# Optimization experiments

Hardware: AMD Instinct MI355X
Metric: run time of the kernel (lower is better)

The kernel has to match this reference:

```python
import jax, jax.numpy as jnp
import numpy as np

F = 64
PASS_STEPS = 3
VAR_N, CON_N, EQ_N = 50000, 50000, 10000
NNZ, EQ_NNZ = 800000, 200000
CONT_SCALE = 0.1  # continuous_var_scale


def _pairnorm(x):
    # PairNorm(subtract_mean=False): x / sqrt(mean_i ||x_i||^2 + eps)
    return x / jnp.sqrt(1e-6 + jnp.mean(jnp.sum(x * x, axis=1)))


def _mlp(x, w1, b1, w2, b2):
    # Linear -> PairNorm -> ReLU -> Linear (fused elementwise chain)
    return jax.nn.relu(_pairnorm(x @ w1 + b1)) @ w2 + b2


def _segsum(vals, idx, n):
    return jax.ops.segment_sum(vals, idx, num_segments=n)


def setup_inputs() -> dict:
    key = jax.random.key(0)
    ks = jax.random.split(key, 32)
    def w(k, i, o):
        return jax.random.normal(k, (i, o), jnp.float32) / np.sqrt(i).astype(np.float32)
    z = lambda n: jnp.zeros((n,), jnp.float32)
    return {
        "ineq_src": jax.random.randint(ks[0], (NNZ,), 0, VAR_N),
        "ineq_dst": jax.random.randint(ks[1], (NNZ,), 0, CON_N),
        "ineq_val": jax.random.normal(ks[2], (NNZ,), jnp.float32),
        "eq_src": jax.random.randint(ks[3], (EQ_NNZ,), 0, VAR_N),
        "eq_dst": jax.random.randint(ks[4], (EQ_NNZ,), 0, EQ_N),
        "eq_val": jax.random.normal(ks[5], (EQ_NNZ,), jnp.float32),
        "const_values": jax.random.normal(ks[6], (CON_N,), jnp.float32),
        "eq_const_values": jax.random.normal(ks[7], (EQ_N,), jnp.float32),
        "relaxed_solution": jax.random.uniform(ks[8], (VAR_N,), jnp.float32),
        "objective_multipliers": jax.random.normal(ks[9], (VAR_N,), jnp.float32),
        "integer_mask": (jax.random.uniform(ks[10], (VAR_N,)) < 0.5).astype(jnp.float32),
        "noise": jax.random.normal(ks[11], (PASS_STEPS, VAR_N, 4), jnp.float32),
        "q_w1": w(ks[12], F + 4, F), "q_b1": z(F),
        "q_w2": w(ks[13], F, F), "q_b2": z(F),
        "cu_w1": w(ks[14], 2 * F, F), "cu_b1": z(F),
        "cu_w2": w(ks[15], F, 2 * F), "cu_b2": z(2 * F),
        "ec_w1": w(ks[16], 2 * F, F), "ec_b1": z(F),
        "ec_w2": w(ks[17], F, 2 * F), "ec_b2": z(2 * F),
        "vu_w1": w(ks[18], 4 * F + 2, F), "vu_b1": z(F),
        "vu_w2": w(ks[19], F, F), "vu_b2": z(F),
        "o_w1": w(ks[20], F, F), "o_b1": z(F),
        "o_w2": w(ks[21], F, 1), "o_b2": z(1),
    }


def reference(ineq_src, ineq_dst, ineq_val, eq_src, eq_dst, eq_val,
              const_values, eq_const_values, relaxed_solution,
              objective_multipliers, integer_mask, noise,
              q_w1, q_b1, q_w2, q_b2, cu_w1, cu_b1, cu_w2, cu_b2,
              ec_w1, ec_b1, ec_w2, ec_b2, vu_w1, vu_b1, vu_w2, vu_b2,
              o_w1, o_b1, o_w2, o_b2):
    var_n = relaxed_solution.shape[0]
    con_n = const_values.shape[0]
    eq_n = eq_const_values.shape[0]
    f = q_w2.shape[1]
    cv = const_values[:, None]
    ecv = eq_const_values[:, None]
    int_mask = integer_mask[:, None]
    obj = objective_multipliers[:, None]
    obj = obj / (jnp.sqrt(jnp.mean(obj * obj)) + 1e-6)

    variables = jnp.ones((var_n, f), ineq_val.dtype) * relaxed_solution[:, None]
    # A^T @ variables and B^T @ variables (bipartite SpMM as gather + segment-sum)
    constraints = _segsum(ineq_val[:, None] * variables[ineq_src], ineq_dst, con_n)
    eq_constraints = _segsum(eq_val[:, None] * variables[eq_src], eq_dst, eq_n)

    val_pos = jax.nn.relu(ineq_val)
    val_neg = jax.nn.relu(-ineq_val)
    const_scaler = jnp.sqrt(_segsum(ineq_val ** 2, ineq_dst, con_n) + 1e-6)[:, None]
    eq_scaler = jnp.sqrt(_segsum(eq_val ** 2, eq_dst, eq_n) + 1e-6)[:, None]
    vars_scaler = jnp.sqrt(_segsum(ineq_val ** 2, ineq_src, var_n) + 1e-6)[:, None]

    outputs = []
    for i in range(noise.shape[0]):  # pass_steps, small fixed count
        query = _mlp(jnp.concatenate([variables, noise[i]], axis=-1), q_w1, q_b1, q_w2, q_b2)
        query = query + 0.5 * int_mask  # (q+0.5)*m + q*(1-m)

        lhs = _segsum(ineq_val[:, None] * query[ineq_src], ineq_dst, con_n)
        const_loss = (lhs - cv) / const_scaler
        const_tmp = _mlp(jnp.concatenate([constraints, const_loss], axis=-1), cu_w1, cu_b1, cu_w2, cu_b2)
        constraints = const_tmp[:, :f] + 0.5 * constraints
        cf = const_tmp[:, f:]
        msg_pos = _segsum(val_pos[:, None] * cf[ineq_dst], ineq_src, var_n) / vars_scaler
        msg_neg = _segsum(val_neg[:, None] * cf[ineq_dst], ineq_src, var_n) / vars_scaler

        eq_lhs = _segsum(eq_val[:, None] * query[eq_src], eq_dst, eq_n)
        eq_loss = jnp.square((ecv - eq_lhs) / eq_scaler)
        eq_tmp = _mlp(jnp.concatenate([eq_constraints, eq_loss], axis=-1), ec_w1, ec_b1, ec_w2, ec_b2)
        eq_constraints = eq_tmp[:, :f] + 0.5 * eq_constraints
        eq2var = _segsum(eq_val[:, None] * eq_tmp[:, f:][eq_dst], eq_src, var_n)

        var_msg = jnp.concatenate([variables, msg_pos, msg_neg, eq2var, obj, int_mask], axis=-1)
        variables = _mlp(var_msg, vu_w1, vu_b1, vu_w2, vu_b2) + 0.5 * variables

        out_vars = _mlp(variables, o_w1, o_b1, o_w2, o_b2)
        # eval mode: no logistic noise injected
        out = jax.nn.sigmoid(out_vars) * int_mask + out_vars * (1.0 - int_mask) * CONT_SCALE
        outputs.append(out)

    return jnp.stack(outputs), out_vars
```

## Files before the change

kernel.cpp:

```cpp
#include <hip/hip_runtime.h>
#include <hip/hip_fp16.h>
#include <math.h>


constexpr int VAR_N = 50000;
constexpr int CON_N = 50000;
constexpr int EQ_N  = 10000;
constexpr int NNZ_I = 800000;
constexpr int NNZ_E = 200000;
constexpr int NPASS = 3;

constexpr int CAP_ID = 48;
constexpr int CAP_IS = 48;
constexpr int CAP_ED = 64;
constexpr int CAP_ES = 24;

typedef _Float16 f16x8 __attribute__((ext_vector_type(8)));
typedef float    f32x4 __attribute__((ext_vector_type(4)));

__device__ __forceinline__ float wred(float v) {
#pragma unroll
  for (int o = 32; o > 0; o >>= 1) v += __shfl_down(v, o, 64);
  return v;
}

__device__ __forceinline__ float unpack_val(unsigned e) {
  return __half2float(__ushort_as_half((unsigned short)(e & 0xFFFFu)));
}

__device__ __forceinline__ unsigned u4get(const uint4& q, int k) {
  return k == 0 ? q.x : (k == 1 ? q.y : (k == 2 ? q.z : q.w));
}

__device__ __forceinline__ float cellsum(const float* p) {
  float s = 0.0f;
#pragma unroll
  for (int i = 0; i < 8; ++i) s += p[i * 16];
  return s;
}

struct PrepArgs {
  const float* src[9];
  int K[9]; int C[9]; int base[9]; int end[9];
};

__global__ __launch_bounds__(256) void prep_wt_k(PrepArgs a, __half* __restrict__ wt)
{
  int idx = blockIdx.x * 256 + threadIdx.x;
  if (idx >= 65536) return;
#pragma unroll
  for (int i = 0; i < 9; ++i) {
    if (idx < a.end[i]) {
      int local = idx - a.base[i];
      int k = local % a.K[i];
      int c = local / a.K[i];
      wt[idx] = __float2half_rn(a.src[i][(size_t)k * a.C[i] + c]);
      return;
    }
  }
}

struct GemmSide {
  const float* X0; const float* X1;
  const __half* WT;
  const float* W;  const float* bias;
  float* out; float* aux;
  const float* ssin; float* ssout; float ssdiv;
  const float* exA; const float* exB; const float* exScale;
  int N; int nblk;
};

template<int K, int COLS, int MODE, int EXTRA, bool RELUNORM, bool OUT_SS, int POSTOP>
__global__ __launch_bounds__(256) void mlp_gemm(GemmSide A, GemmSide B)
{
  constexpr int NCB = COLS / 16;
  constexpr int NS  = K / 32;
  constexpr int KP  = K + 8;
  __shared__ __half Wl[COLS * KP];
  __shared__ float red[4];

  const bool inA = (blockIdx.x < (unsigned)A.nblk);
  const GemmSide& S = inA ? A : B;
  const int bid = blockIdx.x - (inA ? 0 : A.nblk);
  const int nblk = inA ? A.nblk : B.nblk;

  const int tid = threadIdx.x, lane = tid & 63, wid = tid >> 6;
  const int lr = lane & 15;
  const int kgrp = (lane >> 4) * 8;

  for (int idx = tid; idx < COLS * (K / 8); idx += 256) {
    int c = idx / (K / 8), seg = idx % (K / 8);
    *(f16x8*)&Wl[c * KP + seg * 8] = *(const f16x8*)(S.WT + (size_t)c * K + seg * 8);
  }
  __syncthreads();

  float inv_s = 1.0f;
  if constexpr (RELUNORM) inv_s = rsqrtf(1e-6f + cellsum(S.ssin) / S.ssdiv);
  float oscale = 0.0f;
  if constexpr (EXTRA == 2) oscale = 1.0f / (sqrtf((*S.exScale) * (1.0f / VAR_N)) + 1e-6f);

  float bcol[NCB], ew0[NCB], ew1[NCB], ew2[NCB], ew3[NCB];
#pragma unroll
  for (int c = 0; c < NCB; ++c) {
    int col = c * 16 + lr;
    bcol[c] = S.bias[col];
    if constexpr (EXTRA == 1) {
      ew0[c] = S.W[(size_t)(K + 0) * COLS + col];
      ew1[c] = S.W[(size_t)(K + 1) * COLS + col];
      ew2[c] = S.W[(size_t)(K + 2) * COLS + col];
      ew3[c] = S.W[(size_t)(K + 3) * COLS + col];
    }
    if constexpr (EXTRA == 2) {
      ew0[c] = S.W[(size_t)(K + 0) * COLS + col];
      ew1[c] = S.W[(size_t)(K + 1) * COLS + col];
    }
  }

  const int nStrips = (S.N + 15) / 16;
  const int nw = nblk * 4;
  float ssloc = 0.0f;

  for (int strip = bid * 4 + wid; strip < nStrips; strip += nw) {
    const int row0 = strip * 16;
    const int arow = row0 + lr;
    const bool rok = arow < S.N;

    float4 u[NS], v[NS];
#pragma unroll
    for (int s = 0; s < NS; ++s) {
      if (rok) {
        const int gk = s * 32 + kgrp;
        const float* p;
        if constexpr (MODE == 0) p = S.X0 + (size_t)arow * K + gk;
        else p = (gk < 64) ? (S.X0 + ((size_t)arow << 6) + gk)
                           : (S.X1 + (size_t)arow * (K - 64) + (gk - 64));
        u[s] = *(const float4*)p;
        v[s] = *(const float4*)(p + 4);
      } else {
        u[s] = make_float4(0.f, 0.f, 0.f, 0.f);
        v[s] = make_float4(0.f, 0.f, 0.f, 0.f);
      }
    }

    f32x4 acc[NCB] = {};
#pragma unroll
    for (int s = 0; s < NS; ++s) {
      float4 uu = u[s], vv = v[s];
      if constexpr (RELUNORM) {
        uu.x = fmaxf(uu.x, 0.f); uu.y = fmaxf(uu.y, 0.f);
        uu.z = fmaxf(uu.z, 0.f); uu.w = fmaxf(uu.w, 0.f);
        vv.x = fmaxf(vv.x, 0.f); vv.y = fmaxf(vv.y, 0.f);
        vv.z = fmaxf(vv.z, 0.f); vv.w = fmaxf(vv.w, 0.f);
      }
      f16x8 af;
      af[0] = (_Float16)uu.x; af[1] = (_Float16)uu.y;
      af[2] = (_Float16)uu.z; af[3] = (_Float16)uu.w;
      af[4] = (_Float16)vv.x; af[5] = (_Float16)vv.y;
      af[6] = (_Float16)vv.z; af[7] = (_Float16)vv.w;
#pragma unroll
      for (int c = 0; c < NCB; ++c) {
        const f16x8 bf = *(const f16x8*)&Wl[(c * 16 + lr) * KP + s * 32 + kgrp];
        acc[c] = __builtin_amdgcn_mfma_f32_16x16x32_f16(af, bf, acc[c], 0, 0, 0);
      }
    }

#pragma unroll
    for (int j = 0; j < 4; ++j) {
      int grow = row0 + ((lane >> 4) << 2) + j;
      if (grow < S.N) {
        float nx = 0, ny = 0, nz = 0, nw4 = 0, ov = 0, mv = 0;
        if constexpr (EXTRA == 1) {
          float4 n4 = *reinterpret_cast<const float4*>(&S.exA[(size_t)grow * 4]);
          nx = n4.x; ny = n4.y; nz = n4.z; nw4 = n4.w;
        }
        if constexpr (EXTRA == 2) { ov = S.exA[grow] * oscale; mv = S.exB[grow]; }
#pragma unroll
        for (int c = 0; c < NCB; ++c) {
          int col = c * 16 + lr;
          float vv2 = acc[c][j];
          if constexpr (RELUNORM) vv2 *= inv_s;
          vv2 += bcol[c];
          if constexpr (EXTRA == 1)
            vv2 = fmaf(nx, ew0[c], fmaf(ny, ew1[c], fmaf(nz, ew2[c], fmaf(nw4, ew3[c], vv2))));
          if constexpr (EXTRA == 2)
            vv2 = fmaf(ov, ew0[c], fmaf(mv, ew1[c], vv2));
          if constexpr (POSTOP == 1) vv2 += 0.5f * S.aux[grow];
          if constexpr (POSTOP == 2) vv2 += 0.5f * S.aux[((size_t)grow << 6) + col];
          if constexpr (POSTOP == 3) {
            if (col < 64) {
              float nv = vv2 + 0.5f * S.aux[((size_t)grow << 6) + col];
              S.aux[((size_t)grow << 6) + col] = nv;
            } else {
              S.out[((size_t)grow << 6) + (col - 64)] = vv2;
            }
          } else {
            S.out[(size_t)grow * COLS + col] = vv2;
          }
          if constexpr (OUT_SS) ssloc = fmaf(vv2, vv2, ssloc);
        }
      }
    }
  }

  if constexpr (OUT_SS) {
    ssloc = wred(ssloc);
    if (lane == 0) red[wid] = ssloc;
    __syncthreads();
    if (tid == 0) {
      float s = red[0] + red[1] + red[2] + red[3];
      atomicAdd(&S.ssout[(blockIdx.x & 7) * 16], s);
    }
  }
}

constexpr int QI = NNZ_I / 4;
constexpr int QE = NNZ_E / 4;

__global__ __launch_bounds__(256) void build_all_k(
    const int* __restrict__ isrc, const int* __restrict__ idst, const float* __restrict__ ival,
    const int* __restrict__ esrc, const int* __restrict__ edst, const float* __restrict__ evalv,
    int* __restrict__ cntID, unsigned* __restrict__ listID,
    int* __restrict__ cntIS, unsigned* __restrict__ listIS,
    int* __restrict__ cntED, unsigned* __restrict__ listED,
    int* __restrict__ cntES, unsigned* __restrict__ listES)
{
  int t = blockIdx.x * 256 + threadIdx.x;
  if (t < QI) {
    int4   s4 = *(const int4*)(isrc + 4 * t);
    int4   d4 = *(const int4*)(idst + 4 * t);
    float4 v4 = *(const float4*)(ival + 4 * t);
    int   ss[4] = { s4.x, s4.y, s4.z, s4.w };
    int   dd[4] = { d4.x, d4.y, d4.z, d4.w };
    float vv[4] = { v4.x, v4.y, v4.z, v4.w };
    unsigned hb[4]; int pd[4], ps[4];
#pragma unroll
    for (int k = 0; k < 4; ++k) hb[k] = (unsigned)__half_as_ushort(__float2half_rn(vv[k]));
#pragma unroll
    for (int k = 0; k < 4; ++k) pd[k] = atomicAdd(&cntID[dd[k]], 1);
#pragma unroll
    for (int k = 0; k < 4; ++k) ps[k] = atomicAdd(&cntIS[ss[k]], 1);
#pragma unroll
    for (int k = 0; k < 4; ++k)
      if (pd[k] < CAP_ID) listID[(size_t)dd[k] * CAP_ID + pd[k]] = ((unsigned)ss[k] << 16) | hb[k];
#pragma unroll
    for (int k = 0; k < 4; ++k)
      if (ps[k] < CAP_IS) listIS[(size_t)ss[k] * CAP_IS + ps[k]] = ((unsigned)dd[k] << 16) | hb[k];
  } else if (t < QI + QE) {
    int e = t - QI;
    int4   s4 = *(const int4*)(esrc + 4 * e);
    int4   d4 = *(const int4*)(edst + 4 * e);
    float4 v4 = *(const float4*)(evalv + 4 * e);
    int   ss[4] = { s4.x, s4.y, s4.z, s4.w };
    int   dd[4] = { d4.x, d4.y, d4.z, d4.w };
    float vv[4] = { v4.x, v4.y, v4.z, v4.w };
    unsigned hb[4]; int pd[4], ps[4];
#pragma unroll
    for (int k = 0; k < 4; ++k) hb[k] = (unsigned)__half_as_ushort(__float2half_rn(vv[k]));
#pragma unroll
    for (int k = 0; k < 4; ++k) pd[k] = atomicAdd(&cntED[dd[k]], 1);
#pragma unroll
    for (int k = 0; k < 4; ++k) ps[k] = atomicAdd(&cntES[ss[k]], 1);
#pragma unroll
    for (int k = 0; k < 4; ++k)
      if (pd[k] < CAP_ED) listED[(size_t)dd[k] * CAP_ED + pd[k]] = ((unsigned)ss[k] << 16) | hb[k];
#pragma unroll
    for (int k = 0; k < 4; ++k)
      if (ps[k] < CAP_ES) listES[(size_t)ss[k] * CAP_ES + ps[k]] = ((unsigned)dd[k] << 16) | hb[k];
  }
}

__global__ __launch_bounds__(256) void init_rows_k(
    const float* __restrict__ relaxed,
    const int* __restrict__ cntID, const unsigned* __restrict__ listID,
    const int* __restrict__ cntED, const unsigned* __restrict__ listED,
    float* __restrict__ variables, float* __restrict__ constraints, float* __restrict__ eqcons)
{
  int widx = blockIdx.x * 4 + (threadIdx.x >> 6);
  int lane = threadIdx.x & 63;
  if (widx < VAR_N) {
    variables[((size_t)widx << 6) + lane] = relaxed[widx];
  } else if (widx < VAR_N + CON_N) {
    int i = widx - VAR_N;
    int n = min(cntID[i], CAP_ID);
    float t = 0.0f;
    if (lane < n) {
      unsigned e = listID[(size_t)i * CAP_ID + lane];
      t = unpack_val(e) * relaxed[e >> 16];
    }
    t = wred(t);
    t = __shfl(t, 0, 64);
    constraints[((size_t)i << 6) + lane] = t;
  } else if (widx < VAR_N + CON_N + EQ_N) {
    int i = widx - VAR_N - CON_N;
    int n = min(cntED[i], CAP_ED);
    float t = 0.0f;
    if (lane < n) {
      unsigned e = listED[(size_t)i * CAP_ED + lane];
      t = unpack_val(e) * relaxed[e >> 16];
    }
    t = wred(t);
    t = __shfl(t, 0, 64);
    eqcons[((size_t)i << 6) + lane] = t;
  }
}

__global__ __launch_bounds__(256) void gather_loss_k(
    const int* __restrict__ cntC, const unsigned* __restrict__ listC,
    const int* __restrict__ cntE, const unsigned* __restrict__ listE,
    const float* __restrict__ qry,
    const float* __restrict__ cv, const float* __restrict__ ecv,
    float* __restrict__ closs, float* __restrict__ eloss)
{
  constexpr int nbC = (CON_N + 3) / 4;
  int b = blockIdx.x;
  int lane = threadIdx.x & 63;
  if (b < nbC) {
    int i = b * 4 + (threadIdx.x >> 6);
    if (i >= CON_N) return;
    int n = min(cntC[i], CAP_ID);
    const uint4* lst = (const uint4*)(listC + (size_t)i * CAP_ID);
    float acc = 0.0f, ss = 0.0f;
    for (int j4 = 0; j4 * 4 < n; ++j4) {
      uint4 q = lst[j4];
#pragma unroll
      for (int k = 0; k < 4; ++k) {
        int j = j4 * 4 + k;
        if (j < n) {
          unsigned e = u4get(q, k);
          float v = unpack_val(e);
          acc = fmaf(v, qry[((size_t)(e >> 16) << 6) + lane], acc);
          ss  = fmaf(v, v, ss);
        }
      }
    }
    closs[((size_t)i << 6) + lane] = (acc - cv[i]) * rsqrtf(ss + 1e-6f);
  } else {
    int i = (b - nbC) * 4 + (threadIdx.x >> 6);
    if (i >= EQ_N) return;
    int n = min(cntE[i], CAP_ED);
    const uint4* lst = (const uint4*)(listE + (size_t)i * CAP_ED);
    float acc = 0.0f, ss = 0.0f;
    for (int j4 = 0; j4 * 4 < n; ++j4) {
      uint4 q = lst[j4];
#pragma unroll
      for (int k = 0; k < 4; ++k) {
        int j = j4 * 4 + k;
        if (j < n) {
          unsigned e = u4get(q, k);
          float v = unpack_val(e);
          acc = fmaf(v, qry[((size_t)(e >> 16) << 6) + lane], acc);
          ss  = fmaf(v, v, ss);
        }
      }
    }
    float t = (ecv[i] - acc) * rsqrtf(ss + 1e-6f);
    eloss[((size_t)i << 6) + lane] = t * t;
  }
}

__global__ __launch_bounds__(256) void gather_vmsg_k(
    const int* __restrict__ cntS, const unsigned* __restrict__ listS,
    const int* __restrict__ cntES, const unsigned* __restrict__ listES,
    const float* __restrict__ ctmpHi, const float* __restrict__ etmpHi,
    float* __restrict__ msgs)
{
  int i = blockIdx.x * 4 + (threadIdx.x >> 6);
  if (i >= VAR_N) return;
  int lane = threadIdx.x & 63;

  float pos = 0.0f, neg = 0.0f, vss = 0.0f;
  {
    int n = min(cntS[i], CAP_IS);
    const uint4* lst = (const uint4*)(listS + (size_t)i * CAP_IS);
    for (int j4 = 0; j4 * 4 < n; ++j4) {
      uint4 q = lst[j4];
#pragma unroll
      for (int k = 0; k < 4; ++k) {
        int j = j4 * 4 + k;
        if (j < n) {
          unsigned e = u4get(q, k);
          float v = unpack_val(e);
          float c = ctmpHi[((size_t)(e >> 16) << 6) + lane];
          vss = fmaf(v, v, vss);
          if (v > 0.0f) pos = fmaf(v, c, pos);
          else          neg = fmaf(-v, c, neg);
        }
      }
    }
  }
  float e2v = 0.0f;
  {
    int n = min(cntES[i], CAP_ES);
    const uint4* lst = (const uint4*)(listES + (size_t)i * CAP_ES);
    for (int j4 = 0; j4 * 4 < n; ++j4) {
      uint4 q = lst[j4];
#pragma unroll
      for (int k = 0; k < 4; ++k) {
        int j = j4 * 4 + k;
        if (j < n) {
          unsigned e = u4get(q, k);
          e2v = fmaf(unpack_val(e), etmpHi[((size_t)(e >> 16) << 6) + lane], e2v);
        }
      }
    }
  }
  float ivs = rsqrtf(vss + 1e-6f);
  float* row = msgs + (size_t)i * 192;
  row[lane]       = pos * ivs;
  row[64 + lane]  = neg * ivs;
  row[128 + lane] = e2v;
}

__global__ __launch_bounds__(256) void sumsq_k(const float* __restrict__ x, int n, float* out)
{
  float s = 0.0f;
  for (int i = blockIdx.x * 256 + threadIdx.x; i < n; i += gridDim.x * 256) {
    float v = x[i]; s = fmaf(v, v, s);
  }
  s = wred(s);
  __shared__ float red[4];
  int lane = threadIdx.x & 63, wid = threadIdx.x >> 6;
  if (lane == 0) red[wid] = s;
  __syncthreads();
  if (threadIdx.x == 0) atomicAdd(out, red[0] + red[1] + red[2] + red[3]);
}

__global__ __launch_bounds__(256) void out_k(
    const float* __restrict__ H, const float* __restrict__ ssin,
    const float* __restrict__ ow2, const float* __restrict__ ob2,
    const float* __restrict__ mask, float* __restrict__ dout, int pass)
{
  int row = blockIdx.x * 4 + (threadIdx.x >> 6);
  if (row >= VAR_N) return;
  int lane = threadIdx.x & 63;
  float inv_s = rsqrtf(1e-6f + cellsum(ssin) / (float)VAR_N);
  float t = fmaxf(H[(size_t)row * 64 + lane] * inv_s, 0.0f) * ow2[lane];
  t = wred(t);
  if (lane == 0) {
    float ov = t + ob2[0];
    float m = mask[row];
    float sig = 1.0f / (1.0f + expf(-ov));
    dout[pass * VAR_N + row] = sig * m + ov * (1.0f - m) * 0.1f;
    if (pass == NPASS - 1) dout[3 * VAR_N + row] = ov;
  }
}

extern "C" void kernel_launch(void* const* d_in, const int* in_sizes, int n_in,
                              void* d_out, int out_size, void* d_ws, size_t ws_size,
                              hipStream_t stream)
{
  const int*   isrc = (const int*)  d_in[0];
  const int*   idst = (const int*)  d_in[1];
  const float* ival = (const float*)d_in[2];
  const int*   esrc = (const int*)  d_in[3];
  const int*   edst = (const int*)  d_in[4];
  const float* evalv= (const float*)d_in[5];
  const float* cv   = (const float*)d_in[6];
  const float* ecv  = (const float*)d_in[7];
  const float* relaxed = (const float*)d_in[8];
  const float* obj  = (const float*)d_in[9];
  const float* mask = (const float*)d_in[10];
  const float* noise= (const float*)d_in[11];
  const float* q_w1 = (const float*)d_in[12];
  const float* q_b1 = (const float*)d_in[13];
  const float* q_w2 = (const float*)d_in[14];
  const float* q_b2 = (const float*)d_in[15];
  const float* cu_w1= (const float*)d_in[16];
  const float* cu_b1= (const float*)d_in[17];
  const float* cu_w2= (const float*)d_in[18];
  const float* cu_b2= (const float*)d_in[19];
  const float* ec_w1= (const float*)d_in[20];
  const float* ec_b1= (const float*)d_in[21];
  const float* ec_w2= (const float*)d_in[22];
  const float* ec_b2= (const float*)d_in[23];
  const float* vu_w1= (const float*)d_in[24];
  const float* vu_b1= (const float*)d_in[25];
  const float* vu_w2= (const float*)d_in[26];
  const float* vu_b2= (const float*)d_in[27];
  const float* o_w1 = (const float*)d_in[28];
  const float* o_b1 = (const float*)d_in[29];
  const float* o_w2 = (const float*)d_in[30];
  const float* o_b2 = (const float*)d_in[31];
  float* dout = (float*)d_out;
  float* w = (float*)d_ws;

  size_t off = 0;
  auto A = [&](size_t n){ size_t o = off; off += (n + 63) & ~(size_t)63; return o; };
  const size_t oVarA  = A((size_t)VAR_N * 64);
  const size_t oVarB  = A((size_t)VAR_N * 64);
  const size_t oCons  = A((size_t)CON_N * 64);
  const size_t oEqc   = A((size_t)EQ_N  * 64);
  const size_t oQry   = A((size_t)VAR_N * 64);
  const size_t oH     = A((size_t)VAR_N * 64);
  const size_t oHE    = A((size_t)EQ_N  * 64);
  const size_t oCtmp  = A((size_t)CON_N * 64);
  const size_t oEtmp  = A((size_t)EQ_N  * 64);
  const size_t oCloss = A((size_t)CON_N * 64);
  const size_t oEloss = A((size_t)EQ_N  * 64);
  const size_t oMsgs  = A((size_t)VAR_N * 192);
  const size_t oScal  = A(2048);
  const size_t oWT    = A(32768);
  const size_t oCntID = A(CON_N);
  const size_t oCntIS = A(VAR_N);
  const size_t oCntED = A(EQ_N);
  const size_t oCntES = A(VAR_N);
  const size_t oListID = A((size_t)CON_N * CAP_ID);
  const size_t oListIS = A((size_t)VAR_N * CAP_IS);
  const size_t oListED = A((size_t)EQ_N  * CAP_ED);
  const size_t oListES = A((size_t)VAR_N * CAP_ES);

  float* scal = w + oScal;
  __half* wtBase = (__half*)(w + oWT);
  int*  cntID = (int*)(w + oCntID);
  int*  cntIS = (int*)(w + oCntIS);
  int*  cntED = (int*)(w + oCntED);
  int*  cntES = (int*)(w + oCntES);
  unsigned* listID = (unsigned*)(w + oListID);
  unsigned* listIS = (unsigned*)(w + oListIS);
  unsigned* listED = (unsigned*)(w + oListED);
  unsigned* listES = (unsigned*)(w + oListES);

  const int bQ1 = 0,      bQ2 = 4096,  bCU1 = 8192,  bCU2 = 16384, bEC1 = 24576;
  const int bEC2 = 32768, bVU1 = 40960, bVU2 = 57344, bO1 = 61440;

  hipMemsetAsync((void*)(w + oScal), 0, 2048 * 4, stream);
  hipMemsetAsync((void*)(w + oCntID), 0, (oListID - oCntID) * 4, stream);

  {
    PrepArgs pa;
    const float* srcs[9] = { q_w1, q_w2, cu_w1, cu_w2, ec_w1, ec_w2, vu_w1, vu_w2, o_w1 };
    int Ks[9]   = { 64, 64, 128, 64, 128, 64, 256, 64, 64 };
    int Cs[9]   = { 64, 64, 64, 128, 64, 128, 64, 64, 64 };
    int bases[9]= { bQ1, bQ2, bCU1, bCU2, bEC1, bEC2, bVU1, bVU2, bO1 };
    for (int i = 0; i < 9; ++i) {
      pa.src[i] = srcs[i]; pa.K[i] = Ks[i]; pa.C[i] = Cs[i];
      pa.base[i] = bases[i]; pa.end[i] = bases[i] + Ks[i] * Cs[i];
    }
    prep_wt_k<<<(65536 + 255) / 256, 256, 0, stream>>>(pa, wtBase);
  }

  build_all_k<<<(QI + QE + 255) / 256, 256, 0, stream>>>(
      isrc, idst, ival, esrc, edst, evalv,
      cntID, listID, cntIS, listIS, cntED, listED, cntES, listES);
  sumsq_k<<<64, 256, 0, stream>>>(obj, VAR_N, scal);
  init_rows_k<<<(VAR_N + CON_N + EQ_N + 3) / 4, 256, 0, stream>>>(
      relaxed, cntID, listID, cntED, listED, w + oVarA, w + oCons, w + oEqc);

  float* varCur = w + oVarA;
  float* varNxt = w + oVarB;

  GemmSide Z = {};
  const int NBV = 768;
  const int NBC = 640, NBE = 128;

  for (int p = 0; p < NPASS; ++p) {
    float* ssq0 = scal + 16 + (size_t)(p * 5 + 0) * 128;
    float* ssq1 = scal + 16 + (size_t)(p * 5 + 1) * 128;
    float* ssq2 = scal + 16 + (size_t)(p * 5 + 2) * 128;
    float* ssq3 = scal + 16 + (size_t)(p * 5 + 3) * 128;
    float* ssq4 = scal + 16 + (size_t)(p * 5 + 4) * 128;

    {
      GemmSide S = { varCur, nullptr, wtBase + bQ1, q_w1, q_b1, w + oH, nullptr,
                     nullptr, ssq0, 1.0f,
                     noise + (size_t)p * VAR_N * 4, nullptr, nullptr, VAR_N, NBV };
      mlp_gemm<64, 64, 0, 1, false, true, 0><<<NBV, 256, 0, stream>>>(S, Z);
    }
    {
      GemmSide S = { w + oH, nullptr, wtBase + bQ2, q_w2, q_b2, w + oQry, (float*)mask,
                     ssq0, nullptr, (float)VAR_N,
                     nullptr, nullptr, nullptr, VAR_N, NBV };
      mlp_gemm<64, 64, 0, 0, true, false, 1><<<NBV, 256, 0, stream>>>(S, Z);
    }
    gather_loss_k<<<(CON_N + 3) / 4 + (EQ_N + 3) / 4, 256, 0, stream>>>(
        cntID, listID, cntED, listED, w + oQry, cv, ecv, w + oCloss, w + oEloss);
    {
      GemmSide Sa = { w + oCons, w + oCloss, wtBase + bCU1, cu_w1, cu_b1, w + oH, nullptr,
                      nullptr, ssq1, 1.0f, nullptr, nullptr, nullptr, CON_N, NBC };
      GemmSide Sb = { w + oEqc, w + oEloss, wtBase + bEC1, ec_w1, ec_b1, w + oHE, nullptr,
                      nullptr, ssq2, 1.0f, nullptr, nullptr, nullptr, EQ_N, NBE };
      mlp_gemm<128, 64, 1, 0, false, true, 0><<<NBC + NBE, 256, 0, stream>>>(Sa, Sb);
    }
    {
      GemmSide Sa = { w + oH, nullptr, wtBase + bCU2, cu_w2, cu_b2, w + oCtmp, w + oCons,
                      ssq1, nullptr, (float)CON_N, nullptr, nullptr, nullptr, CON_N, NBC };
      GemmSide Sb = { w + oHE, nullptr, wtBase + bEC2, ec_w2, ec_b2, w + oEtmp, w + oEqc,
                      ssq2, nullptr, (float)EQ_N, nullptr, nullptr, nullptr, EQ_N, NBE };
      mlp_gemm<64, 128, 0, 0, true, false, 3><<<NBC + NBE, 256, 0, stream>>>(Sa, Sb);
    }
    gather_vmsg_k<<<(VAR_N + 3) / 4, 256, 0, stream>>>(
        cntIS, listIS, cntES, listES, w + oCtmp, w + oEtmp, w + oMsgs);
    {
      GemmSide S = { varCur, w + oMsgs, wtBase + bVU1, vu_w1, vu_b1, w + oH, nullptr,
                     nullptr, ssq3, 1.0f, obj, mask, scal, VAR_N, NBV };
      mlp_gemm<256, 64, 1, 2, false, true, 0><<<NBV, 256, 0, stream>>>(S, Z);
    }
    {
      GemmSide S = { w + oH, nullptr, wtBase + bVU2, vu_w2, vu_b2, varNxt, varCur,
                     ssq3, nullptr, (float)VAR_N, nullptr, nullptr, nullptr, VAR_N, NBV };
      mlp_gemm<64, 64, 0, 0, true, false, 2><<<NBV, 256, 0, stream>>>(S, Z);
    }
    {
      GemmSide S = { varNxt, nullptr, wtBase + bO1, o_w1, o_b1, w + oH, nullptr,
                     nullptr, ssq4, 1.0f, nullptr, nullptr, nullptr, VAR_N, NBV };
      mlp_gemm<64, 64, 0, 0, false, true, 0><<<NBV, 256, 0, stream>>>(S, Z);
    }
    out_k<<<(VAR_N + 3) / 4, 256, 0, stream>>>(w + oH, ssq4, o_w2, o_b2, mask, dout, p);

    float* t = varCur; varCur = varNxt; varNxt = t;
  }
}
```

Baseline: 1.040 ms.

## Store all intermediate activations in fp16 to halve memory traffic

Changes every intermediate activation buffer (variables, constraints, queries, hidden layers, messages, losses) from fp32 to fp16, so GEMM kernels load f16x8 directly into MFMA operands and the gather kernels read half-width rows. The aim is to cut the bandwidth of the memory-bound gathers and GEMM loads. The edge-list build kernel also changes from four to two edges per thread. The cost is lower precision in the recurrent state and possible overflow or underflow in the fp16 intermediates.

```diff
diff --git a/kernel.cpp b/kernel.cpp
--- a/kernel.cpp
+++ b/kernel.cpp
@@ -17,6 +17,7 @@
 
 typedef _Float16 f16x8 __attribute__((ext_vector_type(8)));
 typedef float    f32x4 __attribute__((ext_vector_type(4)));
+typedef _Float16 half_t;
 
 __device__ __forceinline__ float wred(float v) {
 #pragma unroll
@@ -44,7 +45,7 @@
   int K[9]; int C[9]; int base[9]; int end[9];
 };
 
-__global__ __launch_bounds__(256) void prep_wt_k(PrepArgs a, __half* __restrict__ wt)
+__global__ __launch_bounds__(256) void prep_wt_k(PrepArgs a, half_t* __restrict__ wt)
 {
   int idx = blockIdx.x * 256 + threadIdx.x;
   if (idx >= 65536) return;
@@ -54,17 +55,17 @@
       int local = idx - a.base[i];
       int k = local % a.K[i];
       int c = local / a.K[i];
-      wt[idx] = __float2half_rn(a.src[i][(size_t)k * a.C[i] + c]);
+      wt[idx] = (half_t)a.src[i][(size_t)k * a.C[i] + c];
       return;
     }
   }
 }
 
 struct GemmSide {
-  const float* X0; const float* X1;
-  const __half* WT;
+  const half_t* X0; const half_t* X1;
+  const half_t* WT;
   const float* W;  const float* bias;
-  float* out; float* aux;
+  half_t* out; half_t* auxH; const float* auxF;
   const float* ssin; float* ssout; float ssdiv;
   const float* exA; const float* exB; const float* exScale;
   int N; int nblk;
@@ -76,7 +77,7 @@
   constexpr int NCB = COLS / 16;
   constexpr int NS  = K / 32;
   constexpr int KP  = K + 8;
-  __shared__ __half Wl[COLS * KP];
+  __shared__ half_t Wl[COLS * KP];
   __shared__ float red[4];
 
   const bool inA = (blockIdx.x < (unsigned)A.nblk);
@@ -125,42 +126,33 @@
     const int arow = row0 + lr;
     const bool rok = arow < S.N;
 
-    float4 u[NS], v[NS];
+    f16x8 af[NS];
 #pragma unroll
     for (int s = 0; s < NS; ++s) {
       if (rok) {
         const int gk = s * 32 + kgrp;
-        const float* p;
+        const half_t* p;
         if constexpr (MODE == 0) p = S.X0 + (size_t)arow * K + gk;
         else p = (gk < 64) ? (S.X0 + ((size_t)arow << 6) + gk)
                            : (S.X1 + (size_t)arow * (K - 64) + (gk - 64));
-        u[s] = *(const float4*)p;
-        v[s] = *(const float4*)(p + 4);
+        af[s] = *(const f16x8*)p;
       } else {
-        u[s] = make_float4(0.f, 0.f, 0.f, 0.f);
-        v[s] = make_float4(0.f, 0.f, 0.f, 0.f);
+        af[s] = f16x8{0, 0, 0, 0, 0, 0, 0, 0};
       }
     }
 
     f32x4 acc[NCB] = {};
 #pragma unroll
     for (int s = 0; s < NS; ++s) {
-      float4 uu = u[s], vv = v[s];
+      f16x8 a = af[s];
       if constexpr (RELUNORM) {
-        uu.x = fmaxf(uu.x, 0.f); uu.y = fmaxf(uu.y, 0.f);
-        uu.z = fmaxf(uu.z, 0.f); uu.w = fmaxf(uu.w, 0.f);
-        vv.x = fmaxf(vv.x, 0.f); vv.y = fmaxf(vv.y, 0.f);
-        vv.z = fmaxf(vv.z, 0.f); vv.w = fmaxf(vv.w, 0.f);
-      }
-      f16x8 af;
-      af[0] = (_Float16)uu.x; af[1] = (_Float16)uu.y;
-      af[2] = (_Float16)uu.z; af[3] = (_Float16)uu.w;
-      af[4] = (_Float16)vv.x; af[5] = (_Float16)vv.y;
-      af[6] = (_Float16)vv.z; af[7] = (_Float16)vv.w;
+#pragma unroll
+        for (int i = 0; i < 8; ++i) a[i] = a[i] > (half_t)0 ? a[i] : (half_t)0;
+      }
 #pragma unroll
       for (int c = 0; c < NCB; ++c) {
         const f16x8 bf = *(const f16x8*)&Wl[(c * 16 + lr) * KP + s * 32 + kgrp];
-        acc[c] = __builtin_amdgcn_mfma_f32_16x16x32_f16(af, bf, acc[c], 0, 0, 0);
+        acc[c] = __builtin_amdgcn_mfma_f32_16x16x32_f16(a, bf, acc[c], 0, 0, 0);
       }
     }
 
@@ -184,17 +176,17 @@
             vv2 = fmaf(nx, ew0[c], fmaf(ny, ew1[c], fmaf(nz, ew2[c], fmaf(nw4, ew3[c], vv2))));
           if constexpr (EXTRA == 2)
             vv2 = fmaf(ov, ew0[c], fmaf(mv, ew1[c], vv2));
-          if constexpr (POSTOP == 1) vv2 += 0.5f * S.aux[grow];
-          if constexpr (POSTOP == 2) vv2 += 0.5f * S.aux[((size_t)grow << 6) + col];
+          if constexpr (POSTOP == 1) vv2 += 0.5f * S.auxF[grow];
+          if constexpr (POSTOP == 2) vv2 += 0.5f * (float)S.auxH[((size_t)grow << 6) + col];
           if constexpr (POSTOP == 3) {
             if (col < 64) {
-              float nv = vv2 + 0.5f * S.aux[((size_t)grow << 6) + col];
-              S.aux[((size_t)grow << 6) + col] = nv;
+              float nv = vv2 + 0.5f * (float)S.auxH[((size_t)grow << 6) + col];
+              S.auxH[((size_t)grow << 6) + col] = (half_t)nv;
             } else {
-              S.out[((size_t)grow << 6) + (col - 64)] = vv2;
+              S.out[((size_t)grow << 6) + (col - 64)] = (half_t)vv2;
             }
           } else {
-            S.out[(size_t)grow * COLS + col] = vv2;
+            S.out[(size_t)grow * COLS + col] = (half_t)vv2;
           }
           if constexpr (OUT_SS) ssloc = fmaf(vv2, vv2, ssloc);
         }
@@ -213,8 +205,8 @@
   }
 }
 
-constexpr int QI = NNZ_I / 4;
-constexpr int QE = NNZ_E / 4;
+constexpr int QI2 = NNZ_I / 2;
+constexpr int QE2 = NNZ_E / 2;
 
 __global__ __launch_bounds__(256) void build_all_k(
     const int* __restrict__ isrc, const int* __restrict__ idst, const float* __restrict__ ival,
@@ -225,46 +217,46 @@
     int* __restrict__ cntES, unsigned* __restrict__ listES)
 {
   int t = blockIdx.x * 256 + threadIdx.x;
-  if (t < QI) {
-    int4   s4 = *(const int4*)(isrc + 4 * t);
-    int4   d4 = *(const int4*)(idst + 4 * t);
-    float4 v4 = *(const float4*)(ival + 4 * t);
-    int   ss[4] = { s4.x, s4.y, s4.z, s4.w };
-    int   dd[4] = { d4.x, d4.y, d4.z, d4.w };
-    float vv[4] = { v4.x, v4.y, v4.z, v4.w };
-    unsigned hb[4]; int pd[4], ps[4];
-#pragma unroll
-    for (int k = 0; k < 4; ++k) hb[k] = (unsigned)__half_as_ushort(__float2half_rn(vv[k]));
-#pragma unroll
-    for (int k = 0; k < 4; ++k) pd[k] = atomicAdd(&cntID[dd[k]], 1);
-#pragma unroll
-    for (int k = 0; k < 4; ++k) ps[k] = atomicAdd(&cntIS[ss[k]], 1);
-#pragma unroll
-    for (int k = 0; k < 4; ++k)
+  if (t < QI2) {
+    int2   s2 = *(const int2*)(isrc + 2 * t);
+    int2   d2 = *(const int2*)(idst + 2 * t);
+    float2 v2 = *(const float2*)(ival + 2 * t);
+    int   ss[2] = { s2.x, s2.y };
+    int   dd[2] = { d2.x, d2.y };
+    float vv[2] = { v2.x, v2.y };
+    unsigned hb[2]; int pd[2], ps[2];
+#pragma unroll
+    for (int k = 0; k < 2; ++k) hb[k] = (unsigned)__half_as_ushort(__float2half_rn(vv[k]));
+#pragma unroll
+    for (int k = 0; k < 2; ++k) pd[k] = atomicAdd(&cntID[dd[k]], 1);
+#pragma unroll
+    for (int k = 0; k < 2; ++k) ps[k] = atomicAdd(&cntIS[ss[k]], 1);
+#pragma unroll
+    for (int k = 0; k < 2; ++k)
       if (pd[k] < CAP_ID) listID[(size_t)dd[k] * CAP_ID + pd[k]] = ((unsigned)ss[k] << 16) | hb[k];
 #pragma unroll
-    for (int k = 0; k < 4; ++k)
+    for (int k = 0; k < 2; ++k)
       if (ps[k] < CAP_IS) listIS[(size_t)ss[k] * CAP_IS + ps[k]] = ((unsigned)dd[k] << 16) | hb[k];
-  } else if (t < QI + QE) {
-    int e = t - QI;
-    int4   s4 = *(const int4*)(esrc + 4 * e);
-    int4   d4 = *(const int4*)(edst + 4 * e);
-    float4 v4 = *(const float4*)(evalv + 4 * e);
-    int   ss[4] = { s4.x, s4.y, s4.z, s4.w };
-    int   dd[4] = { d4.x, d4.y, d4.z, d4.w };
-    float vv[4] = { v4.x, v4.y, v4.z, v4.w };
-    unsigned hb[4]; int pd[4], ps[4];
-#pragma unroll
-    for (int k = 0; k < 4; ++k) hb[k] = (unsigned)__half_as_ushort(__float2half_rn(vv[k]));
-#pragma unroll
-    for (int k = 0; k < 4; ++k) pd[k] = atomicAdd(&cntED[dd[k]], 1);
-#pragma unroll
-    for (int k = 0; k < 4; ++k) ps[k] = atomicAdd(&cntES[ss[k]], 1);
-#pragma unroll
-    for (int k = 0; k < 4; ++k)
+  } else if (t < QI2 + QE2) {
+    int e = t - QI2;
+    int2   s2 = *(const int2*)(esrc + 2 * e);
+    int2   d2 = *(const int2*)(edst + 2 * e);
+    float2 v2 = *(const float2*)(evalv + 2 * e);
+    int   ss[2] = { s2.x, s2.y };
+    int   dd[2] = { d2.x, d2.y };
+    float vv[2] = { v2.x, v2.y };
+    unsigned hb[2]; int pd[2], ps[2];
+#pragma unroll
+    for (int k = 0; k < 2; ++k) hb[k] = (unsigned)__half_as_ushort(__float2half_rn(vv[k]));
+#pragma unroll
+    for (int k = 0; k < 2; ++k) pd[k] = atomicAdd(&cntED[dd[k]], 1);
+#pragma unroll
+    for (int k = 0; k < 2; ++k) ps[k] = atomicAdd(&cntES[ss[k]], 1);
+#pragma unroll
+    for (int k = 0; k < 2; ++k)
       if (pd[k] < CAP_ED) listED[(size_t)dd[k] * CAP_ED + pd[k]] = ((unsigned)ss[k] << 16) | hb[k];
 #pragma unroll
-    for (int k = 0; k < 4; ++k)
+    for (int k = 0; k < 2; ++k)
       if (ps[k] < CAP_ES) listES[(size_t)ss[k] * CAP_ES + ps[k]] = ((unsigned)dd[k] << 16) | hb[k];
   }
 }
@@ -273,12 +265,12 @@
     const float* __restrict__ relaxed,
     const int* __restrict__ cntID, const unsigned* __restrict__ listID,
     const int* __restrict__ cntED, const unsigned* __restrict__ listED,
-    float* __restrict__ variables, float* __restrict__ constraints, float* __restrict__ eqcons)
+    half_t* __restrict__ variables, half_t* __restrict__ constraints, half_t* __restrict__ eqcons)
 {
   int widx = blockIdx.x * 4 + (threadIdx.x >> 6);
   int lane = threadIdx.x & 63;
   if (widx < VAR_N) {
-    variables[((size_t)widx << 6) + lane] = relaxed[widx];
+    variables[((size_t)widx << 6) + lane] = (half_t)relaxed[widx];
   } else if (widx < VAR_N + CON_N) {
     int i = widx - VAR_N;
     int n = min(cntID[i], CAP_ID);
@@ -289,7 +281,7 @@
     }
     t = wred(t);
     t = __shfl(t, 0, 64);
-    constraints[((size_t)i << 6) + lane] = t;
+    constraints[((size_t)i << 6) + lane] = (half_t)t;
   } else if (widx < VAR_N + CON_N + EQ_N) {
     int i = widx - VAR_N - CON_N;
     int n = min(cntED[i], CAP_ED);
@@ -300,16 +292,16 @@
     }
     t = wred(t);
     t = __shfl(t, 0, 64);
-    eqcons[((size_t)i << 6) + lane] = t;
+    eqcons[((size_t)i << 6) + lane] = (half_t)t;
   }
 }
 
 __global__ __launch_bounds__(256) void gather_loss_k(
     const int* __restrict__ cntC, const unsigned* __restrict__ listC,
     const int* __restrict__ cntE, const unsigned* __restrict__ listE,
-    const float* __restrict__ qry,
+    const half_t* __restrict__ qry,
     const float* __restrict__ cv, const float* __restrict__ ecv,
-    float* __restrict__ closs, float* __restrict__ eloss)
+    half_t* __restrict__ closs, half_t* __restrict__ eloss)
 {
   constexpr int nbC = (CON_N + 3) / 4;
   int b = blockIdx.x;
@@ -328,12 +320,12 @@
         if (j < n) {
           unsigned e = u4get(q, k);
           float v = unpack_val(e);
-          acc = fmaf(v, qry[((size_t)(e >> 16) << 6) + lane], acc);
+          acc = fmaf(v, (float)qry[((size_t)(e >> 16) << 6) + lane], acc);
           ss  = fmaf(v, v, ss);
         }
       }
     }
-    closs[((size_t)i << 6) + lane] = (acc - cv[i]) * rsqrtf(ss + 1e-6f);
+    closs[((size_t)i << 6) + lane] = (half_t)((acc - cv[i]) * rsqrtf(ss + 1e-6f));
   } else {
     int i = (b - nbC) * 4 + (threadIdx.x >> 6);
     if (i >= EQ_N) return;
@@ -348,21 +340,21 @@
         if (j < n) {
           unsigned e = u4get(q, k);
           float v = unpack_val(e);
-          acc = fmaf(v, qry[((size_t)(e >> 16) << 6) + lane], acc);
+          acc = fmaf(v, (float)qry[((size_t)(e >> 16) << 6) + lane], acc);
           ss  = fmaf(v, v, ss);
         }
       }
     }
     float t = (ecv[i] - acc) * rsqrtf(ss + 1e-6f);
-    eloss[((size_t)i << 6) + lane] = t * t;
+    eloss[((size_t)i << 6) + lane] = (half_t)(t * t);
   }
 }
 
 __global__ __launch_bounds__(256) void gather_vmsg_k(
     const int* __restrict__ cntS, const unsigned* __restrict__ listS,
     const int* __restrict__ cntES, const unsigned* __restrict__ listES,
-    const float* __restrict__ ctmpHi, const float* __restrict__ etmpHi,
-    float* __restrict__ msgs)
+    const half_t* __restrict__ ctmpHi, const half_t* __restrict__ etmpHi,
+    half_t* __restrict__ msgs)
 {
   int i = blockIdx.x * 4 + (threadIdx.x >> 6);
   if (i >= VAR_N) return;
@@ -380,7 +372,7 @@
         if (j < n) {
           unsigned e = u4get(q, k);
           float v = unpack_val(e);
-          float c = ctmpHi[((size_t)(e >> 16) << 6) + lane];
+          float c = (float)ctmpHi[((size_t)(e >> 16) << 6) + lane];
           vss = fmaf(v, v, vss);
           if (v > 0.0f) pos = fmaf(v, c, pos);
           else          neg = fmaf(-v, c, neg);
@@ -399,16 +391,16 @@
         int j = j4 * 4 + k;
         if (j < n) {
           unsigned e = u4get(q, k);
-          e2v = fmaf(unpack_val(e), etmpHi[((size_t)(e >> 16) << 6) + lane], e2v);
+          e2v = fmaf(unpack_val(e), (float)etmpHi[((size_t)(e >> 16) << 6) + lane], e2v);
         }
       }
     }
   }
   float ivs = rsqrtf(vss + 1e-6f);
-  float* row = msgs + (size_t)i * 192;
-  row[lane]       = pos * ivs;
-  row[64 + lane]  = neg * ivs;
-  row[128 + lane] = e2v;
+  half_t* row = msgs + (size_t)i * 192;
+  row[lane]       = (half_t)(pos * ivs);
+  row[64 + lane]  = (half_t)(neg * ivs);
+  row[128 + lane] = (half_t)e2v;
 }
 
 __global__ __launch_bounds__(256) void sumsq_k(const float* __restrict__ x, int n, float* out)
@@ -426,7 +418,7 @@
 }
 
 __global__ __launch_bounds__(256) void out_k(
-    const float* __restrict__ H, const float* __restrict__ ssin,
+    const half_t* __restrict__ H, const float* __restrict__ ssin,
     const float* __restrict__ ow2, const float* __restrict__ ob2,
     const float* __restrict__ mask, float* __restrict__ dout, int pass)
 {
@@ -434,7 +426,7 @@
   if (row >= VAR_N) return;
   int lane = threadIdx.x & 63;
   float inv_s = rsqrtf(1e-6f + cellsum(ssin) / (float)VAR_N);
-  float t = fmaxf(H[(size_t)row * 64 + lane] * inv_s, 0.0f) * ow2[lane];
+  float t = fmaxf((float)H[(size_t)row * 64 + lane] * inv_s, 0.0f) * ow2[lane];
   t = wred(t);
   if (lane == 0) {
     float ov = t + ob2[0];
@@ -510,7 +502,7 @@
   const size_t oListES = A((size_t)VAR_N * CAP_ES);
 
   float* scal = w + oScal;
-  __half* wtBase = (__half*)(w + oWT);
+  half_t* wtBase = (half_t*)(w + oWT);
   int*  cntID = (int*)(w + oCntID);
   int*  cntIS = (int*)(w + oCntIS);
   int*  cntED = (int*)(w + oCntED);
@@ -519,6 +511,19 @@
   unsigned* listIS = (unsigned*)(w + oListIS);
   unsigned* listED = (unsigned*)(w + oListED);
   unsigned* listES = (unsigned*)(w + oListES);
+
+  half_t* hVarA  = (half_t*)(w + oVarA);
+  half_t* hVarB  = (half_t*)(w + oVarB);
+  half_t* hCons  = (half_t*)(w + oCons);
+  half_t* hEqc   = (half_t*)(w + oEqc);
+  half_t* hQry   = (half_t*)(w + oQry);
+  half_t* hH     = (half_t*)(w + oH);
+  half_t* hHE    = (half_t*)(w + oHE);
+  half_t* hCtmp  = (half_t*)(w + oCtmp);
+  half_t* hEtmp  = (half_t*)(w + oEtmp);
+  half_t* hCloss = (half_t*)(w + oCloss);
+  half_t* hEloss = (half_t*)(w + oEloss);
+  half_t* hMsgs  = (half_t*)(w + oMsgs);
 
   const int bQ1 = 0,      bQ2 = 4096,  bCU1 = 8192,  bCU2 = 16384, bEC1 = 24576;
   const int bEC2 = 32768, bVU1 = 40960, bVU2 = 57344, bO1 = 61440;
@@ -539,15 +544,15 @@
     prep_wt_k<<<(65536 + 255) / 256, 256, 0, stream>>>(pa, wtBase);
   }
 
-  build_all_k<<<(QI + QE + 255) / 256, 256, 0, stream>>>(
+  build_all_k<<<(QI2 + QE2 + 255) / 256, 256, 0, stream>>>(
       isrc, idst, ival, esrc, edst, evalv,
       cntID, listID, cntIS, listIS, cntED, listED, cntES, listES);
   sumsq_k<<<64, 256, 0, stream>>>(obj, VAR_N, scal);
   init_rows_k<<<(VAR_N + CON_N + EQ_N + 3) / 4, 256, 0, stream>>>(
-      relaxed, cntID, listID, cntED, listED, w + oVarA, w + oCons, w + oEqc);
-
-  float* varCur = w + oVarA;
-  float* varNxt = w + oVarB;
+      relaxed, cntID, listID, cntED, listED, hVarA, hCons, hEqc);
+
+  half_t* varCur = hVarA;
+  half_t* varNxt = hVarB;
 
   GemmSide Z = {};
   const int NBV = 768;
@@ -561,52 +566,52 @@
     float* ssq4 = scal + 16 + (size_t)(p * 5 + 4) * 128;
 
     {
-      GemmSide S = { varCur, nullptr, wtBase + bQ1, q_w1, q_b1, w + oH, nullptr,
+      GemmSide S = { varCur, nullptr, wtBase + bQ1, q_w1, q_b1, hH, nullptr, nullptr,
                      nullptr, ssq0, 1.0f,
                      noise + (size_t)p * VAR_N * 4, nullptr, nullptr, VAR_N, NBV };
       mlp_gemm<64, 64, 0, 1, false, true, 0><<<NBV, 256, 0, stream>>>(S, Z);
     }
     {
-      GemmSide S = { w + oH, nullptr, wtBase + bQ2, q_w2, q_b2, w + oQry, (float*)mask,
+      GemmSide S = { hH, nullptr, wtBase + bQ2, q_w2, q_b2, hQry, nullptr, mask,
                      ssq0, nullptr, (float)VAR_N,
                      nullptr, nullptr, nullptr, VAR_N, NBV };
       mlp_gemm<64, 64, 0, 0, true, false, 1><<<NBV, 256, 0, stream>>>(S, Z);
     }
     gather_loss_k<<<(CON_N + 3) / 4 + (EQ_N + 3) / 4, 256, 0, stream>>>(
-        cntID, listID, cntED, listED, w + oQry, cv, ecv, w + oCloss, w + oEloss);
+        cntID, listID, cntED, listED, hQry, cv, ecv, hCloss, hEloss);
     {
-      GemmSide Sa = { w + oCons, w + oCloss, wtBase + bCU1, cu_w1, cu_b1, w + oH, nullptr,
+      GemmSide Sa = { hCons, hCloss, wtBase + bCU1, cu_w1, cu_b1, hH, nullptr, nullptr,
                       nullptr, ssq1, 1.0f, nullptr, nullptr, nullptr, CON_N, NBC };
-      GemmSide Sb = { w + oEqc, w + oEloss, wtBase + bEC1, ec_w1, ec_b1, w + oHE, nullptr,
+      GemmSide Sb = { hEqc, hEloss, wtBase + bEC1, ec_w1, ec_b1, hHE, nullptr, nullptr,
                       nullptr, ssq2, 1.0f, nullptr, nullptr, nullptr, EQ_N, NBE };
       mlp_gemm<128, 64, 1, 0, false, true, 0><<<NBC + NBE, 256, 0, stream>>>(Sa, Sb);
     }
     {
-      GemmSide Sa = { w + oH, nullptr, wtBase + bCU2, cu_w2, cu_b2, w + oCtmp, w + oCons,
+      GemmSide Sa = { hH, nullptr, wtBase + bCU2, cu_w2, cu_b2, hCtmp, hCons, nullptr,
                       ssq1, nullptr, (float)CON_N, nullptr, nullptr, nullptr, CON_N, NBC };
-      GemmSide Sb = { w + oHE, nullptr, wtBase + bEC2, ec_w2, ec_b2, w + oEtmp, w + oEqc,
+      GemmSide Sb = { hHE, nullptr, wtBase + bEC2, ec_w2, ec_b2, hEtmp, hEqc, nullptr,
                       ssq2, nullptr, (float)EQ_N, nullptr, nullptr, nullptr, EQ_N, NBE };
       mlp_gemm<64, 128, 0, 0, true, false, 3><<<NBC + NBE, 256, 0, stream>>>(Sa, Sb);
     }
     gather_vmsg_k<<<(VAR_N + 3) / 4, 256, 0, stream>>>(
-        cntIS, listIS, cntES, listES, w + oCtmp, w + oEtmp, w + oMsgs);
+        cntIS, listIS, cntES, listES, hCtmp, hEtmp, hMsgs);
     {
-      GemmSide S = { varCur, w + oMsgs, wtBase + bVU1, vu_w1, vu_b1, w + oH, nullptr,
+      GemmSide S = { varCur, hMsgs, wtBase + bVU1, vu_w1, vu_b1, hH, nullptr, nullptr,
                      nullptr, ssq3, 1.0f, obj, mask, scal, VAR_N, NBV };
       mlp_gemm<256, 64, 1, 2, false, true, 0><<<NBV, 256, 0, stream>>>(S, Z);
     }
     {
-      GemmSide S = { w + oH, nullptr, wtBase + bVU2, vu_w2, vu_b2, varNxt, varCur,
+      GemmSide S = { hH, nullptr, wtBase + bVU2, vu_w2, vu_b2, varNxt, varCur, nullptr,
                      ssq3, nullptr, (float)VAR_N, nullptr, nullptr, nullptr, VAR_N, NBV };
       mlp_gemm<64, 64, 0, 0, true, false, 2><<<NBV, 256, 0, stream>>>(S, Z);
     }
     {
-      GemmSide S = { varNxt, nullptr, wtBase + bO1, o_w1, o_b1, w + oH, nullptr,
+      GemmSide S = { varNxt, nullptr, wtBase + bO1, o_w1, o_b1, hH, nullptr, nullptr,
                      nullptr, ssq4, 1.0f, nullptr, nullptr, nullptr, VAR_N, NBV };
       mlp_gemm<64, 64, 0, 0, false, true, 0><<<NBV, 256, 0, stream>>>(S, Z);
     }
-    out_k<<<(VAR_N + 3) / 4, 256, 0, stream>>>(w + oH, ssq4, o_w2, o_b2, mask, dout, p);
-
-    float* t = varCur; varCur = varNxt; varNxt = t;
-  }
-}
+    out_k<<<(VAR_N + 3) / 4, 256, 0, stream>>>(hH, ssq4, o_w2, o_b2, mask, dout, p);
+
+    half_t* t = varCur; varCur = varNxt; varNxt = t;
+  }
+}
```

New measurement: 947.1 us. -8.9%, faster.
